# Kernel tuning notes

Measured on AMD Instinct MI355X. Metric: run time of the kernel, lower is better.

## Reference

```python
import jax, jax.numpy as jnp
import numpy as np

BN_EPS = 1e-5


def setup_inputs() -> dict:
    key = jax.random.key(0)
    ks = jax.random.split(key, 12)
    N, F, H, E, ED, G, EMB = 59392, 116, 256, 950272, 5, 8, 16
    return {
        "x": jax.random.normal(ks[0], (N, F), dtype=jnp.float32),
        "edge_index": jax.random.randint(ks[1], (2, E), 0, N, dtype=jnp.int64),
        "edge_attr": jax.random.normal(ks[2], (E, ED), dtype=jnp.float32),
        "group_ids": jax.random.randint(ks[3], (N,), 0, G, dtype=jnp.int64),
        "group_emb": jax.random.normal(ks[4], (G, EMB), dtype=jnp.float32),
        "W_in": jax.random.normal(ks[5], (F + EMB, H), dtype=jnp.float32) * 0.05,
        "b_in": jnp.zeros((H,), dtype=jnp.float32),
        "gamma": jnp.ones((H,), dtype=jnp.float32),
        "beta": jnp.zeros((H,), dtype=jnp.float32),
        "We": jax.random.normal(ks[6], (ED, H), dtype=jnp.float32) * 0.05,
        "be": jnp.zeros((H,), dtype=jnp.float32),
        "W1": jax.random.normal(ks[7], (H, H), dtype=jnp.float32) * 0.05,
        "b1": jnp.zeros((H,), dtype=jnp.float32),
        "W2": jax.random.normal(ks[8], (H, H), dtype=jnp.float32) * 0.05,
        "b2": jnp.zeros((H,), dtype=jnp.float32),
    }


def reference(x, edge_index, edge_attr, group_ids, group_emb, W_in, b_in,
              gamma, beta, We, be, W1, b1, W2, b2):
    N = x.shape[0]
    # group-embedding concat (dropout is identity in eval mode)
    h = jnp.concatenate([x, group_emb[group_ids]], axis=-1)      # [N, F+EMB]
    # dynamically-created Linear + ReLU
    h = jax.nn.relu(h @ W_in + b_in)                              # [N, H]
    # BatchNorm over nodes (training stats, biased var)
    mu = jnp.mean(h, axis=0)
    var = jnp.mean(jnp.square(h - mu), axis=0)
    h = (h - mu) * jax.lax.rsqrt(var + BN_EPS) * gamma + beta
    # GINEConv: msg = ReLU(x_j + lin(edge_attr)); sum-aggregate at target
    src, dst = edge_index[0], edge_index[1]
    msg = jax.nn.relu(h[src] + edge_attr @ We + be)               # [E, H]
    agg = jax.ops.segment_sum(msg, dst, num_segments=N)          # [N, H]
    z = h + agg                                                   # (1+eps)*h, eps=0
    out = jax.nn.relu(z @ W1 + b1) @ W2 + b2                      # 2-layer MLP
    out = jax.nn.relu(out)
    return (out, edge_attr)
```

## Files before the change

### kernel.cpp

```cpp
#include <hip/hip_runtime.h>
#include <hip/hip_bf16.h>
#include <cstdint>
#include <cstddef>

#define H 256
#define EMB 16
#define ED 5
#define BN_EPS 1e-5f

typedef __attribute__((ext_vector_type(8))) short short8;
typedef __attribute__((ext_vector_type(4))) float f32x4;
typedef _Float16 h2 __attribute__((ext_vector_type(2)));

__device__ __forceinline__ unsigned short f2bf(float f) {
  unsigned int u = __float_as_uint(f);
  unsigned int r = (u + 0x7fffu + ((u >> 16) & 1u)) >> 16;
  return (unsigned short)r;
}
__device__ __forceinline__ unsigned int pk2bf(float a, float b) {
  return (unsigned int)f2bf(a) | ((unsigned int)f2bf(b) << 16);
}
__device__ __forceinline__ float bfhi(unsigned int u) {
  return __uint_as_float(u & 0xffff0000u);
}
__device__ __forceinline__ float bflo(unsigned int u) {
  return __uint_as_float(u << 16);
}
__device__ __forceinline__ h2 u2h2(unsigned int u) {
  union { unsigned int u; h2 h; } c;
  c.u = u;
  return c.h;
}
__device__ __forceinline__ unsigned int h22u(h2 h) {
  union { h2 h; unsigned int u; } c;
  c.h = h;
  return c.u;
}
__device__ __forceinline__ h2 mkh2(float a, float b) {
  h2 r;
  r.x = (_Float16)a;
  r.y = (_Float16)b;
  return r;
}

__global__ __launch_bounds__(256) void prep_kernel(
    const float* __restrict__ Win, const float* __restrict__ W1,
    const float* __restrict__ W2, const float* __restrict__ gemb,
    const float* __restrict__ b_in, unsigned short* __restrict__ Wtx,
    unsigned short* __restrict__ Wt1, unsigned short* __restrict__ Wt2,
    float* __restrict__ T, float* __restrict__ stats, int* __restrict__ deg,
    int N, int F, int G) {
  int idx = blockIdx.x * 256 + threadIdx.x;
  if (idx < 1024) stats[idx] = 0.f;
  if (idx < N) deg[idx] = 0;
  if (idx < 256 * 128) {
    int n = idx >> 7, k = idx & 127;
    Wtx[idx] = f2bf((k < F) ? Win[(size_t)k * H + n] : 0.f);
  } else if (idx < 256 * 128 + 65536) {
    int i2 = idx - 256 * 128;
    int n = i2 >> 8, k = i2 & 255;
    Wt1[i2] = f2bf(W1[(size_t)k * H + n]);
  } else if (idx < 256 * 128 + 131072) {
    int i2 = idx - 256 * 128 - 65536;
    int n = i2 >> 8, k = i2 & 255;
    Wt2[i2] = f2bf(W2[(size_t)k * H + n]);
  } else if (idx < 256 * 128 + 131072 + G * 256) {
    int i2 = idx - 256 * 128 - 131072;
    int g = i2 >> 8, c = i2 & 255;
    float s = b_in[c];
    #pragma unroll
    for (int k = 0; k < EMB; ++k)
      s = fmaf(gemb[g * EMB + k], Win[(size_t)(F + k) * H + c], s);
    T[i2] = s;
  }
}

__global__ __launch_bounds__(256) void gemm_in_kernel(
    const float* __restrict__ x, const int* __restrict__ gid,
    const unsigned short* __restrict__ Wtx, const float* __restrict__ T,
    unsigned short* __restrict__ h0, float* __restrict__ stats, int F) {
  const int m0 = blockIdx.y * 128;
  const int n0 = blockIdx.x * 128;
  const int tid = threadIdx.x;
  const int lane = tid & 63;
  const int wave = tid >> 6;
  const int wm = (wave & 1) * 64;
  const int wn = (wave >> 1) * 64;
  const int l16 = lane & 15;
  const int quad = lane >> 4;
  __shared__ __align__(16) unsigned short As[128][40];
  __shared__ __align__(16) unsigned short Bs[128][40];
  __shared__ float cs[128], css[128];
  if (tid < 128) {
    cs[tid] = 0.f;
    css[tid] = 0.f;
  }
  f32x4 acc[4][4] = {};
  const int srow = tid >> 1;
  const int half = tid & 1;
  for (int k0 = 0; k0 < 128; k0 += 32) {
    __syncthreads();
    {
      const float* xp = x + (size_t)(m0 + srow) * F;
      float4 xv[4];
      #pragma unroll
      for (int f = 0; f < 4; ++f) {
        int c = k0 + half * 16 + f * 4;
        xv[f] = (c < F) ? *(const float4*)(xp + c)
                        : make_float4(0.f, 0.f, 0.f, 0.f);
      }
      uint4 p0, p1;
      p0.x = pk2bf(xv[0].x, xv[0].y); p0.y = pk2bf(xv[0].z, xv[0].w);
      p0.z = pk2bf(xv[1].x, xv[1].y); p0.w = pk2bf(xv[1].z, xv[1].w);
      p1.x = pk2bf(xv[2].x, xv[2].y); p1.y = pk2bf(xv[2].z, xv[2].w);
      p1.z = pk2bf(xv[3].x, xv[3].y); p1.w = pk2bf(xv[3].z, xv[3].w);
      *(uint4*)(&As[srow][half * 16]) = p0;
      *(uint4*)(&As[srow][half * 16 + 8]) = p1;
    }
    {
      const unsigned short* wp = Wtx + (size_t)(n0 + srow) * 128 + k0 + half * 16;
      *(uint4*)(&Bs[srow][half * 16]) = *(const uint4*)wp;
      *(uint4*)(&Bs[srow][half * 16 + 8]) = *(const uint4*)(wp + 8);
    }
    __syncthreads();
    short8 af[4], bf[4];
    #pragma unroll
    for (int i = 0; i < 4; ++i)
      af[i] = *(const short8*)(&As[wm + i * 16 + l16][quad * 8]);
    #pragma unroll
    for (int j = 0; j < 4; ++j)
      bf[j] = *(const short8*)(&Bs[wn + j * 16 + l16][quad * 8]);
    #pragma unroll
    for (int i = 0; i < 4; ++i)
      #pragma unroll
      for (int j = 0; j < 4; ++j)
        acc[i][j] = __builtin_amdgcn_mfma_f32_16x16x32_bf16(af[i], bf[j],
                                                            acc[i][j], 0, 0, 0);
  }
  int gi[4][4];
  #pragma unroll
  for (int i = 0; i < 4; ++i)
    #pragma unroll
    for (int r = 0; r < 4; ++r)
      gi[i][r] = gid[m0 + wm + i * 16 + quad * 4 + r];
  float ls[4] = {}, lss[4] = {};
  #pragma unroll
  for (int j = 0; j < 4; ++j) {
    const int col = n0 + wn + j * 16 + l16;
    #pragma unroll
    for (int i = 0; i < 4; ++i) {
      #pragma unroll
      for (int r = 0; r < 4; ++r) {
        const int row = m0 + wm + i * 16 + quad * 4 + r;
        float v = fmaxf(acc[i][j][r] + T[gi[i][r] * H + col], 0.f);
        h0[(size_t)row * H + col] = f2bf(v);
        ls[j] += v;
        lss[j] = fmaf(v, v, lss[j]);
      }
    }
  }
  #pragma unroll
  for (int j = 0; j < 4; ++j) {
    const int lc = wn + j * 16 + l16;
    atomicAdd(&cs[lc], ls[j]);
    atomicAdd(&css[lc], lss[j]);
  }
  __syncthreads();
  if (tid < 128) {
    atomicAdd(&stats[n0 + tid], cs[tid]);
    atomicAdd(&stats[H + n0 + tid], css[tid]);
  }
}

__global__ __launch_bounds__(256) void mlp_kernel(
    const unsigned short* __restrict__ z, const unsigned short* __restrict__ Wt1,
    const unsigned short* __restrict__ Wt2, const float* __restrict__ b1,
    const float* __restrict__ b2, float* __restrict__ out) {
  const int m0 = blockIdx.x * 64;
  const int tid = threadIdx.x;
  const int lane = tid & 63;
  const int wave = tid >> 6;
  const int wn = wave * 64;
  const int l16 = lane & 15;
  const int quad = lane >> 4;
  __shared__ __align__(16) unsigned short As[64][40];
  __shared__ __align__(16) unsigned short Bs[256][40];
  __shared__ __align__(16) unsigned short hidS[64][264];
  f32x4 acc[4][4] = {};
  const int ar = tid >> 2, ac = tid & 3;
  for (int k0 = 0; k0 < 256; k0 += 32) {
    __syncthreads();
    *(float4*)(&As[ar][ac * 8]) =
        *(const float4*)(z + (size_t)(m0 + ar) * H + k0 + ac * 8);
    #pragma unroll
    for (int t = 0; t < 4; ++t) {
      int r = ar + t * 64;
      *(float4*)(&Bs[r][ac * 8]) =
          *(const float4*)(Wt1 + (size_t)r * H + k0 + ac * 8);
    }
    __syncthreads();
    short8 af[4], bf[4];
    #pragma unroll
    for (int i = 0; i < 4; ++i)
      af[i] = *(const short8*)(&As[i * 16 + l16][quad * 8]);
    #pragma unroll
    for (int j = 0; j < 4; ++j)
      bf[j] = *(const short8*)(&Bs[wn + j * 16 + l16][quad * 8]);
    #pragma unroll
    for (int i = 0; i < 4; ++i)
      #pragma unroll
      for (int j = 0; j < 4; ++j)
        acc[i][j] = __builtin_amdgcn_mfma_f32_16x16x32_bf16(af[i], bf[j],
                                                            acc[i][j], 0, 0, 0);
  }
  #pragma unroll
  for (int j = 0; j < 4; ++j) {
    const int col = wn + j * 16 + l16;
    const float bj = b1[col];
    #pragma unroll
    for (int i = 0; i < 4; ++i)
      #pragma unroll
      for (int r = 0; r < 4; ++r) {
        const int row = i * 16 + quad * 4 + r;
        hidS[row][col] = f2bf(fmaxf(acc[i][j][r] + bj, 0.f));
      }
  }
  #pragma unroll
  for (int i = 0; i < 4; ++i)
    #pragma unroll
    for (int j = 0; j < 4; ++j)
      acc[i][j] = (f32x4){0.f, 0.f, 0.f, 0.f};
  for (int k0 = 0; k0 < 256; k0 += 32) {
    __syncthreads();
    #pragma unroll
    for (int t = 0; t < 4; ++t) {
      int r = ar + t * 64;
      *(float4*)(&Bs[r][ac * 8]) =
          *(const float4*)(Wt2 + (size_t)r * H + k0 + ac * 8);
    }
    __syncthreads();
    short8 af[4], bf[4];
    #pragma unroll
    for (int i = 0; i < 4; ++i)
      af[i] = *(const short8*)(&hidS[i * 16 + l16][k0 + quad * 8]);
    #pragma unroll
    for (int j = 0; j < 4; ++j)
      bf[j] = *(const short8*)(&Bs[wn + j * 16 + l16][quad * 8]);
    #pragma unroll
    for (int i = 0; i < 4; ++i)
      #pragma unroll
      for (int j = 0; j < 4; ++j)
        acc[i][j] = __builtin_amdgcn_mfma_f32_16x16x32_bf16(af[i], bf[j],
                                                            acc[i][j], 0, 0, 0);
  }
  #pragma unroll
  for (int j = 0; j < 4; ++j) {
    const int col = wn + j * 16 + l16;
    const float bj = b2[col];
    #pragma unroll
    for (int i = 0; i < 4; ++i)
      #pragma unroll
      for (int r = 0; r < 4; ++r) {
        const int row = m0 + i * 16 + quad * 4 + r;
        out[(size_t)row * H + col] = fmaxf(acc[i][j][r] + bj, 0.f);
      }
  }
}

__global__ __launch_bounds__(256) void hbn_kernel(
    const unsigned short* __restrict__ h0, const float* __restrict__ stats,
    const float* __restrict__ gamma, const float* __restrict__ beta,
    const float* __restrict__ be, unsigned short* __restrict__ hbn,
    float inv_n) {
  __shared__ float sa[H], sb[H];
  {
    const int j = threadIdx.x;
    const float mu = stats[j] * inv_n;
    const float var = stats[H + j] * inv_n - mu * mu;
    const float rs = 1.0f / sqrtf(var + BN_EPS);
    const float a = gamma[j] * rs;
    sa[j] = a;
    sb[j] = beta[j] - mu * a + be[j];
  }
  __syncthreads();
  const size_t i = (size_t)blockIdx.x * 256 + threadIdx.x;
  const int c = ((int)(i & 31)) * 8;
  const uint4 hv = ((const uint4*)h0)[i];
  float r[8] = {bflo(hv.x), bfhi(hv.x), bflo(hv.y), bfhi(hv.y),
                bflo(hv.z), bfhi(hv.z), bflo(hv.w), bfhi(hv.w)};
  float o[8];
  #pragma unroll
  for (int t = 0; t < 8; ++t)
    o[t] = fmaf(sa[c + t], r[t], sb[c + t]);
  uint4 ov;
  ov.x = h22u(mkh2(o[0], o[1]));
  ov.y = h22u(mkh2(o[2], o[3]));
  ov.z = h22u(mkh2(o[4], o[5]));
  ov.w = h22u(mkh2(o[6], o[7]));
  ((uint4*)hbn)[i] = ov;
}

__global__ __launch_bounds__(256) void csr_count_kernel(
    const int* __restrict__ ei, int* __restrict__ deg, int E) {
  int e = blockIdx.x * 256 + threadIdx.x;
  if (e < E) atomicAdd(&deg[ei[E + e]], 1);
}

__global__ __launch_bounds__(256) void scan_blocks_kernel(
    const int* __restrict__ deg, int* __restrict__ excl,
    int* __restrict__ bsums, int n) {
  const int tid = threadIdx.x;
  const int i = blockIdx.x * 256 + tid;
  const int lane = tid & 63, wid = tid >> 6;
  int v = (i < n) ? deg[i] : 0;
  int x = v;
  #pragma unroll
  for (int d = 1; d < 64; d <<= 1) {
    int y = __shfl_up(x, d, 64);
    if (lane >= d) x += y;
  }
  __shared__ int ws[4], wo[4];
  if (lane == 63) ws[wid] = x;
  __syncthreads();
  if (tid == 0) {
    int a = 0;
    #pragma unroll
    for (int w = 0; w < 4; ++w) { wo[w] = a; a += ws[w]; }
    bsums[blockIdx.x] = a;
  }
  __syncthreads();
  if (i < n) excl[i] = x - v + wo[wid];
}

__global__ __launch_bounds__(256) void scan_finish_kernel(
    int* __restrict__ row_start, int* __restrict__ cursor,
    const int* __restrict__ bsums, int n, int E, int NB) {
  const int tid = threadIdx.x;
  const int b = blockIdx.x;
  int v = (tid < b && tid < NB) ? bsums[tid] : 0;
  int s = v;
  #pragma unroll
  for (int d = 32; d > 0; d >>= 1) s += __shfl_down(s, d, 64);
  __shared__ int ws[4];
  if ((tid & 63) == 0) ws[tid >> 6] = s;
  __syncthreads();
  const int S = ws[0] + ws[1] + ws[2] + ws[3];
  const int i = b * 256 + tid;
  if (i < n) {
    int r = row_start[i] + S;
    row_start[i] = r;
    cursor[i] = r;
  }
  if (b == 0 && tid == 0) row_start[n] = E;
}

__global__ __launch_bounds__(256) void csr_scatter_kernel(
    const int* __restrict__ ei, const float* __restrict__ ea,
    int* __restrict__ cursor, uint4* __restrict__ rec,
    float* __restrict__ ea_out, int E) {
  int e = blockIdx.x * 256 + threadIdx.x;
  if (e >= E) return;
  int s = ei[e];
  int d = ei[E + e];
  int p = atomicAdd(&cursor[d], 1);
  const float* eap = ea + (size_t)e * ED;
  const float e0 = eap[0], e1 = eap[1], e2 = eap[2], e3 = eap[3], e4 = eap[4];
  uint4 r;
  r.x = (unsigned)s;
  r.y = h22u(mkh2(e0, e1));
  r.z = h22u(mkh2(e2, e3));
  r.w = h22u(mkh2(e4, 0.f));
  rec[p] = r;
  float* op = ea_out + (size_t)e * ED;
  op[0] = e0; op[1] = e1; op[2] = e2; op[3] = e3; op[4] = e4;
}

__device__ __forceinline__ void edge_accum(
    const uint4 rr, const uint2 hv, const h2 wA[5], const h2 wB[5],
    float& ax, float& ay, float& az, float& aw) {
  h2 m01 = u2h2(hv.x);
  h2 m23 = u2h2(hv.y);
  const h2 e01 = u2h2(rr.y), e23 = u2h2(rr.z), e44 = u2h2(rr.w);
  h2 t;
  t.x = e01.x; t.y = e01.x;  m01 += t * wA[0]; m23 += t * wB[0];
  t.x = e01.y; t.y = e01.y;  m01 += t * wA[1]; m23 += t * wB[1];
  t.x = e23.x; t.y = e23.x;  m01 += t * wA[2]; m23 += t * wB[2];
  t.x = e23.y; t.y = e23.y;  m01 += t * wA[3]; m23 += t * wB[3];
  t.x = e44.x; t.y = e44.x;  m01 += t * wA[4]; m23 += t * wB[4];
  const h2 z2 = {(_Float16)0.f, (_Float16)0.f};
  m01 = __builtin_elementwise_max(m01, z2);
  m23 = __builtin_elementwise_max(m23, z2);
  ax += (float)m01.x;
  ay += (float)m01.y;
  az += (float)m23.x;
  aw += (float)m23.y;
}

__global__ __launch_bounds__(256) void aggregate_kernel(
    const unsigned short* __restrict__ hbn, const uint4* __restrict__ rec,
    const float* __restrict__ We, const float* __restrict__ be,
    const int* __restrict__ row_start, unsigned short* __restrict__ z,
    int N) {
  const int lane = threadIdx.x & 63;
  int n = blockIdx.x * 4 + (threadIdx.x >> 6);
  if (n >= N) return;
  n = __builtin_amdgcn_readfirstlane(n);
  const int c = lane * 4;
  const float4 be4 = *(const float4*)(be + c);
  h2 wA[5], wB[5];
  #pragma unroll
  for (int k = 0; k < 5; ++k) {
    wA[k] = mkh2(We[k * H + c], We[k * H + c + 1]);
    wB[k] = mkh2(We[k * H + c + 2], We[k * H + c + 3]);
  }
  float ax = 0.f, ay = 0.f, az = 0.f, aw = 0.f;
  const int s0 = __builtin_amdgcn_readfirstlane(row_start[n]);
  const int s1 = __builtin_amdgcn_readfirstlane(row_start[n + 1]);
  const uint4* rp = rec + s0;
  const int cnt = s1 - s0;
  int i = 0;
  for (; i + 8 <= cnt; i += 8) {
    uint4 rr[8];
    uint2 hh[8];
    #pragma unroll
    for (int u = 0; u < 8; ++u) rr[u] = rp[i + u];
    #pragma unroll
    for (int u = 0; u < 8; ++u)
      hh[u] = *(const uint2*)(hbn + (size_t)(int)rr[u].x * H + c);
    #pragma unroll
    for (int u = 0; u < 8; ++u)
      edge_accum(rr[u], hh[u], wA, wB, ax, ay, az, aw);
  }
  for (; i + 4 <= cnt; i += 4) {
    uint4 rr[4];
    uint2 hh[4];
    #pragma unroll
    for (int u = 0; u < 4; ++u) rr[u] = rp[i + u];
    #pragma unroll
    for (int u = 0; u < 4; ++u)
      hh[u] = *(const uint2*)(hbn + (size_t)(int)rr[u].x * H + c);
    #pragma unroll
    for (int u = 0; u < 4; ++u)
      edge_accum(rr[u], hh[u], wA, wB, ax, ay, az, aw);
  }
  for (; i < cnt; ++i) {
    const uint4 r0 = rp[i];
    const uint2 h0v = *(const uint2*)(hbn + (size_t)(int)r0.x * H + c);
    edge_accum(r0, h0v, wA, wB, ax, ay, az, aw);
  }
  const uint2 hs = *(const uint2*)(hbn + (size_t)n * H + c);
  const h2 hsA = u2h2(hs.x), hsB = u2h2(hs.y);
  float zx = (float)hsA.x - be4.x + ax;
  float zy = (float)hsA.y - be4.y + ay;
  float zz = (float)hsB.x - be4.z + az;
  float zw = (float)hsB.y - be4.w + aw;
  uint2 o;
  o.x = pk2bf(zx, zy);
  o.y = pk2bf(zz, zw);
  *(uint2*)(z + (size_t)n * H + c) = o;
}

extern "C" void kernel_launch(void* const* d_in, const int* in_sizes, int n_in,
                              void* d_out, int out_size, void* d_ws, size_t ws_size,
                              hipStream_t stream) {
  const float* x     = (const float*)d_in[0];
  const int*   ei    = (const int*)d_in[1];
  const float* ea    = (const float*)d_in[2];
  const int*   gid   = (const int*)d_in[3];
  const float* gemb  = (const float*)d_in[4];
  const float* W_in  = (const float*)d_in[5];
  const float* b_in  = (const float*)d_in[6];
  const float* gamma = (const float*)d_in[7];
  const float* beta  = (const float*)d_in[8];
  const float* We    = (const float*)d_in[9];
  const float* be    = (const float*)d_in[10];
  const float* W1    = (const float*)d_in[11];
  const float* b1    = (const float*)d_in[12];
  const float* W2    = (const float*)d_in[13];
  const float* b2    = (const float*)d_in[14];
  float* out = (float*)d_out;

  const int N = in_sizes[3];
  const int E = in_sizes[1] / 2;
  const int F = in_sizes[0] / N;
  const int G = in_sizes[4] / EMB;
  const int NB = (N + 255) / 256;

  char* p = (char*)d_ws;
  auto take = [&](size_t bytes) {
    char* r = p;
    p += (bytes + 255) & ~(size_t)255;
    return r;
  };
  float* stats          = (float*)take(1024 * sizeof(float));
  int* deg              = (int*)take((size_t)N * 4);
  int* row_start        = (int*)take((size_t)(N + 1) * 4);
  int* cursor           = (int*)take((size_t)N * 4);
  int* bsums            = (int*)take((size_t)NB * 4);
  uint4* rec            = (uint4*)take((size_t)E * 16);
  unsigned short* Wtx   = (unsigned short*)take((size_t)256 * 128 * 2);
  unsigned short* Wt1   = (unsigned short*)take((size_t)H * H * 2);
  unsigned short* Wt2   = (unsigned short*)take((size_t)H * H * 2);
  float* T              = (float*)take((size_t)G * H * 4);
  unsigned short* h0    = (unsigned short*)take((size_t)N * H * 2);
  unsigned short* hbn   = (unsigned short*)take((size_t)N * H * 2);
  unsigned short* z     = (unsigned short*)take((size_t)N * H * 2);

  {
    int total = 256 * 128 + 131072 + G * 256;
    int nb = (total + 255) / 256;
    if (nb < (N + 255) / 256) nb = (N + 255) / 256;
    prep_kernel<<<nb, 256, 0, stream>>>(W_in, W1, W2, gemb, b_in, Wtx, Wt1,
                                        Wt2, T, stats, deg, N, F, G);
  }

  csr_count_kernel<<<(E + 255) / 256, 256, 0, stream>>>(ei, deg, E);
  scan_blocks_kernel<<<NB, 256, 0, stream>>>(deg, row_start, bsums, N);
  scan_finish_kernel<<<NB, 256, 0, stream>>>(row_start, cursor, bsums, N, E, NB);
  csr_scatter_kernel<<<(E + 255) / 256, 256, 0, stream>>>(
      ei, ea, cursor, rec, out + (size_t)N * H, E);

  dim3 ggrid(H / 128, N / 128);
  gemm_in_kernel<<<ggrid, 256, 0, stream>>>(x, gid, Wtx, T, h0, stats, F);

  hbn_kernel<<<((size_t)N * H / 8) / 256, 256, 0, stream>>>(
      h0, stats, gamma, beta, be, hbn, 1.0f / (float)N);

  aggregate_kernel<<<(N + 3) / 4, 256, 0, stream>>>(hbn, rec, We, be,
                                                    row_start, z, N);

  mlp_kernel<<<N / 64, 256, 0, stream>>>(z, Wt1, Wt2, b1, b2, out);
}
```

Measured before the change: 391.6 us.

## Split each node's edge list across two waves and pre-shift source offsets

The aggregate kernel now gives each destination node two wavefronts, each handling half of its incoming edges, and sums the partials through shared memory before writing z. The CSR record stores the source index pre-multiplied by the row byte stride, which removes the 64-bit multiply in the gather address. The tail loops are replaced by one clamped, predicated 8-wide loop. This aims to raise memory-level parallelism and shorten the serial per-node chain, at the cost of a block barrier, shared-memory traffic, wasted clamped loads and twice as many waves.

```diff
diff --git a/kernel.cpp b/kernel.cpp
--- a/kernel.cpp
+++ b/kernel.cpp
@@ -366,7 +366,7 @@
   const float* eap = ea + (size_t)e * ED;
   const float e0 = eap[0], e1 = eap[1], e2 = eap[2], e3 = eap[3], e4 = eap[4];
   uint4 r;
-  r.x = (unsigned)s;
+  r.x = ((unsigned)s) << 9;
   r.y = h22u(mkh2(e0, e1));
   r.z = h22u(mkh2(e2, e3));
   r.w = h22u(mkh2(e4, 0.f));
@@ -401,12 +401,16 @@
     const float* __restrict__ We, const float* __restrict__ be,
     const int* __restrict__ row_start, unsigned short* __restrict__ z,
     int N) {
-  const int lane = threadIdx.x & 63;
-  int n = blockIdx.x * 4 + (threadIdx.x >> 6);
-  if (n >= N) return;
-  n = __builtin_amdgcn_readfirstlane(n);
+  __shared__ float sAgg[2][256];
+  const int tid = threadIdx.x;
+  const int lane = tid & 63;
+  const int wave = tid >> 6;
+  const int nl = wave >> 1;
+  const int half = wave & 1;
+  const int n0 = blockIdx.x * 2 + nl;
+  const int n = __builtin_amdgcn_readfirstlane((n0 < N) ? n0 : (N - 1));
   const int c = lane * 4;
-  const float4 be4 = *(const float4*)(be + c);
+  const int c2 = c << 1;
   h2 wA[5], wB[5];
   #pragma unroll
   for (int k = 0; k < 5; ++k) {
@@ -416,48 +420,48 @@
   float ax = 0.f, ay = 0.f, az = 0.f, aw = 0.f;
   const int s0 = __builtin_amdgcn_readfirstlane(row_start[n]);
   const int s1 = __builtin_amdgcn_readfirstlane(row_start[n + 1]);
+  const int cnt = s1 - s0;
+  const int mid = cnt >> 1;
+  int i = half ? mid : 0;
+  const int e = half ? cnt : mid;
   const uint4* rp = rec + s0;
-  const int cnt = s1 - s0;
-  int i = 0;
-  for (; i + 8 <= cnt; i += 8) {
+  const char* hb = (const char*)hbn;
+  for (; i < e; i += 8) {
     uint4 rr[8];
     uint2 hh[8];
     #pragma unroll
-    for (int u = 0; u < 8; ++u) rr[u] = rp[i + u];
+    for (int u = 0; u < 8; ++u) {
+      int idx = i + u;
+      idx = (idx < e) ? idx : (e - 1);
+      rr[u] = rp[idx];
+    }
     #pragma unroll
     for (int u = 0; u < 8; ++u)
-      hh[u] = *(const uint2*)(hbn + (size_t)(int)rr[u].x * H + c);
+      hh[u] = *(const uint2*)(hb + rr[u].x + c2);
+    asm volatile("" ::: "memory");
     #pragma unroll
     for (int u = 0; u < 8; ++u)
-      edge_accum(rr[u], hh[u], wA, wB, ax, ay, az, aw);
-  }
-  for (; i + 4 <= cnt; i += 4) {
-    uint4 rr[4];
-    uint2 hh[4];
-    #pragma unroll
-    for (int u = 0; u < 4; ++u) rr[u] = rp[i + u];
-    #pragma unroll
-    for (int u = 0; u < 4; ++u)
-      hh[u] = *(const uint2*)(hbn + (size_t)(int)rr[u].x * H + c);
-    #pragma unroll
-    for (int u = 0; u < 4; ++u)
-      edge_accum(rr[u], hh[u], wA, wB, ax, ay, az, aw);
-  }
-  for (; i < cnt; ++i) {
-    const uint4 r0 = rp[i];
-    const uint2 h0v = *(const uint2*)(hbn + (size_t)(int)r0.x * H + c);
-    edge_accum(r0, h0v, wA, wB, ax, ay, az, aw);
-  }
-  const uint2 hs = *(const uint2*)(hbn + (size_t)n * H + c);
-  const h2 hsA = u2h2(hs.x), hsB = u2h2(hs.y);
-  float zx = (float)hsA.x - be4.x + ax;
-  float zy = (float)hsA.y - be4.y + ay;
-  float zz = (float)hsB.x - be4.z + az;
-  float zw = (float)hsB.y - be4.w + aw;
-  uint2 o;
-  o.x = pk2bf(zx, zy);
-  o.y = pk2bf(zz, zw);
-  *(uint2*)(z + (size_t)n * H + c) = o;
+      if (i + u < e)
+        edge_accum(rr[u], hh[u], wA, wB, ax, ay, az, aw);
+  }
+  if (half) {
+    *(float4*)(&sAgg[nl][c]) = make_float4(ax, ay, az, aw);
+  }
+  __syncthreads();
+  if (!half && n0 < N) {
+    const float4 p = *(const float4*)(&sAgg[nl][c]);
+    const float4 be4 = *(const float4*)(be + c);
+    const uint2 hs = *(const uint2*)(hbn + (size_t)n * H + c);
+    const h2 hsA = u2h2(hs.x), hsB = u2h2(hs.y);
+    const float zx = (float)hsA.x - be4.x + ax + p.x;
+    const float zy = (float)hsA.y - be4.y + ay + p.y;
+    const float zz = (float)hsB.x - be4.z + az + p.z;
+    const float zw = (float)hsB.y - be4.w + aw + p.w;
+    uint2 o;
+    o.x = pk2bf(zx, zy);
+    o.y = pk2bf(zz, zw);
+    *(uint2*)(z + (size_t)n * H + c) = o;
+  }
 }
 
 extern "C" void kernel_launch(void* const* d_in, const int* in_sizes, int n_in,
@@ -526,7 +530,7 @@
   hbn_kernel<<<((size_t)N * H / 8) / 256, 256, 0, stream>>>(
       h0, stats, gamma, beta, be, hbn, 1.0f / (float)N);
 
-  aggregate_kernel<<<(N + 3) / 4, 256, 0, stream>>>(hbn, rec, We, be,
+  aggregate_kernel<<<(N + 1) / 2, 256, 0, stream>>>(hbn, rec, We, be,
                                                     row_start, z, N);
 
   mlp_kernel<<<N / 64, 256, 0, stream>>>(z, Wt1, Wt2, b1, b2, out);
```

Measured after the change: 435.6 us. +11.2%, slower.

## Software-pipeline edge gathers and precompute byte offsets in aggregate kernel

Applied to the files above, without the earlier changes.

The CSR scatter now stores each source index as a byte offset (index shifted by 9, i.e. times 512 bytes per row), so gather addresses in the aggregate kernel need no multiply or 64-bit conversion. The aggregate loop is double-buffered: the next batch of 8 records and feature gathers is issued before computing the current batch, with scheduling barriers to keep loads ahead of the math. A vector-zero trick forces vector loads for row_start and the records. This is meant to hide gather latency at the cost of more registers; the shifted offsets fit in 32 bits only because N*512 is below 2^32.

```diff
diff --git a/kernel.cpp b/kernel.cpp
--- a/kernel.cpp
+++ b/kernel.cpp
@@ -366,7 +366,7 @@
   const float* eap = ea + (size_t)e * ED;
   const float e0 = eap[0], e1 = eap[1], e2 = eap[2], e3 = eap[3], e4 = eap[4];
   uint4 r;
-  r.x = (unsigned)s;
+  r.x = ((unsigned)s) << 9;
   r.y = h22u(mkh2(e0, e1));
   r.z = h22u(mkh2(e2, e3));
   r.w = h22u(mkh2(e4, 0.f));
@@ -396,6 +396,19 @@
   aw += (float)m23.y;
 }
 
+#define LOADB8(rr, hh, base)                                      \
+  {                                                               \
+    _Pragma("unroll") for (int u = 0; u < 8; ++u)                 \
+        rr[u] = rp[(base) + u];                                   \
+    _Pragma("unroll") for (int u = 0; u < 8; ++u)                 \
+        hh[u] = *(const uint2*)(hb + rr[u].x + c2);               \
+  }
+#define COMP8(rr, hh)                                             \
+  {                                                               \
+    _Pragma("unroll") for (int u = 0; u < 8; ++u)                 \
+        edge_accum(rr[u], hh[u], wA, wB, ax, ay, az, aw);         \
+  }
+
 __global__ __launch_bounds__(256) void aggregate_kernel(
     const unsigned short* __restrict__ hbn, const uint4* __restrict__ rec,
     const float* __restrict__ We, const float* __restrict__ be,
@@ -406,6 +419,9 @@
   if (n >= N) return;
   n = __builtin_amdgcn_readfirstlane(n);
   const int c = lane * 4;
+  const int c2 = c << 1;
+  int vzero;
+  asm("v_mov_b32 %0, 0" : "=v"(vzero));
   const float4 be4 = *(const float4*)(be + c);
   h2 wA[5], wB[5];
   #pragma unroll
@@ -414,22 +430,32 @@
     wB[k] = mkh2(We[k * H + c + 2], We[k * H + c + 3]);
   }
   float ax = 0.f, ay = 0.f, az = 0.f, aw = 0.f;
-  const int s0 = __builtin_amdgcn_readfirstlane(row_start[n]);
-  const int s1 = __builtin_amdgcn_readfirstlane(row_start[n + 1]);
-  const uint4* rp = rec + s0;
+  const int2 rs2 = *(const int2*)(row_start + n + vzero);
+  const int s0 = __builtin_amdgcn_readfirstlane(rs2.x);
+  const int s1 = __builtin_amdgcn_readfirstlane(rs2.y);
   const int cnt = s1 - s0;
-  int i = 0;
-  for (; i + 8 <= cnt; i += 8) {
-    uint4 rr[8];
-    uint2 hh[8];
-    #pragma unroll
-    for (int u = 0; u < 8; ++u) rr[u] = rp[i + u];
-    #pragma unroll
-    for (int u = 0; u < 8; ++u)
-      hh[u] = *(const uint2*)(hbn + (size_t)(int)rr[u].x * H + c);
-    #pragma unroll
-    for (int u = 0; u < 8; ++u)
-      edge_accum(rr[u], hh[u], wA, wB, ax, ay, az, aw);
+  const uint4* rp = rec + s0 + vzero;
+  const char* hb = (const char*)hbn;
+  const int nb = cnt >> 3;
+  int i = nb << 3;
+  if (nb > 0) {
+    uint4 rrA[8], rrB[8];
+    uint2 hhA[8], hhB[8];
+    LOADB8(rrA, hhA, 0);
+    for (int b = 1; b < nb; ++b) {
+      if (b & 1) {
+        LOADB8(rrB, hhB, b << 3);
+        __builtin_amdgcn_sched_barrier(0);
+        COMP8(rrA, hhA);
+      } else {
+        LOADB8(rrA, hhA, b << 3);
+        __builtin_amdgcn_sched_barrier(0);
+        COMP8(rrB, hhB);
+      }
+    }
+    __builtin_amdgcn_sched_barrier(0);
+    if (nb & 1) { COMP8(rrA, hhA); }
+    else        { COMP8(rrB, hhB); }
   }
   for (; i + 4 <= cnt; i += 4) {
     uint4 rr[4];
@@ -438,14 +464,14 @@
     for (int u = 0; u < 4; ++u) rr[u] = rp[i + u];
     #pragma unroll
     for (int u = 0; u < 4; ++u)
-      hh[u] = *(const uint2*)(hbn + (size_t)(int)rr[u].x * H + c);
+      hh[u] = *(const uint2*)(hb + rr[u].x + c2);
     #pragma unroll
     for (int u = 0; u < 4; ++u)
       edge_accum(rr[u], hh[u], wA, wB, ax, ay, az, aw);
   }
   for (; i < cnt; ++i) {
     const uint4 r0 = rp[i];
-    const uint2 h0v = *(const uint2*)(hbn + (size_t)(int)r0.x * H + c);
+    const uint2 h0v = *(const uint2*)(hb + r0.x + c2);
     edge_accum(r0, h0v, wA, wB, ax, ay, az, aw);
   }
   const uint2 hs = *(const uint2*)(hbn + (size_t)n * H + c);
```

After: 462.9 us. 18.2% more time.

## Fuse BatchNorm apply into edge aggregation and drop the hbn pass

Applied to the files above, without the earlier changes.

Removes the separate hbn kernel. gemm_in now stores h0 in fp16, and aggregate_kernel recomputes the per-column BN scale and shift from stats and applies them to each gathered neighbour row on the fly. That saves a full N×H read and write plus one launch, at the cost of a few extra fp16 FMAs per edge. The edge record now holds a pre-shifted byte offset to drop address arithmetic, and the edge_attr output copy moves out of the scatter kernel into a separate vectorised copy kernel. Applying the affine in fp16 on fp16-stored h0 may change numerics slightly.

```diff
diff --git a/kernel.cpp b/kernel.cpp
--- a/kernel.cpp
+++ b/kernel.cpp
@@ -20,11 +20,10 @@
 __device__ __forceinline__ unsigned int pk2bf(float a, float b) {
   return (unsigned int)f2bf(a) | ((unsigned int)f2bf(b) << 16);
 }
-__device__ __forceinline__ float bfhi(unsigned int u) {
-  return __uint_as_float(u & 0xffff0000u);
-}
-__device__ __forceinline__ float bflo(unsigned int u) {
-  return __uint_as_float(u << 16);
+__device__ __forceinline__ unsigned short f2h(float f) {
+  union { _Float16 h; unsigned short u; } c;
+  c.h = (_Float16)f;
+  return c.u;
 }
 __device__ __forceinline__ h2 u2h2(unsigned int u) {
   union { unsigned int u; h2 h; } c;
@@ -153,7 +152,7 @@
       for (int r = 0; r < 4; ++r) {
         const int row = m0 + wm + i * 16 + quad * 4 + r;
         float v = fmaxf(acc[i][j][r] + T[gi[i][r] * H + col], 0.f);
-        h0[(size_t)row * H + col] = f2bf(v);
+        h0[(size_t)row * H + col] = f2h(v);
         ls[j] += v;
         lss[j] = fmaf(v, v, lss[j]);
       }
@@ -267,39 +266,6 @@
   }
 }
 
-__global__ __launch_bounds__(256) void hbn_kernel(
-    const unsigned short* __restrict__ h0, const float* __restrict__ stats,
-    const float* __restrict__ gamma, const float* __restrict__ beta,
-    const float* __restrict__ be, unsigned short* __restrict__ hbn,
-    float inv_n) {
-  __shared__ float sa[H], sb[H];
-  {
-    const int j = threadIdx.x;
-    const float mu = stats[j] * inv_n;
-    const float var = stats[H + j] * inv_n - mu * mu;
-    const float rs = 1.0f / sqrtf(var + BN_EPS);
-    const float a = gamma[j] * rs;
-    sa[j] = a;
-    sb[j] = beta[j] - mu * a + be[j];
-  }
-  __syncthreads();
-  const size_t i = (size_t)blockIdx.x * 256 + threadIdx.x;
-  const int c = ((int)(i & 31)) * 8;
-  const uint4 hv = ((const uint4*)h0)[i];
-  float r[8] = {bflo(hv.x), bfhi(hv.x), bflo(hv.y), bfhi(hv.y),
-                bflo(hv.z), bfhi(hv.z), bflo(hv.w), bfhi(hv.w)};
-  float o[8];
-  #pragma unroll
-  for (int t = 0; t < 8; ++t)
-    o[t] = fmaf(sa[c + t], r[t], sb[c + t]);
-  uint4 ov;
-  ov.x = h22u(mkh2(o[0], o[1]));
-  ov.y = h22u(mkh2(o[2], o[3]));
-  ov.z = h22u(mkh2(o[4], o[5]));
-  ov.w = h22u(mkh2(o[6], o[7]));
-  ((uint4*)hbn)[i] = ov;
-}
-
 __global__ __launch_bounds__(256) void csr_count_kernel(
     const int* __restrict__ ei, int* __restrict__ deg, int E) {
   int e = blockIdx.x * 256 + threadIdx.x;
@@ -356,8 +322,7 @@
 
 __global__ __launch_bounds__(256) void csr_scatter_kernel(
     const int* __restrict__ ei, const float* __restrict__ ea,
-    int* __restrict__ cursor, uint4* __restrict__ rec,
-    float* __restrict__ ea_out, int E) {
+    int* __restrict__ cursor, uint4* __restrict__ rec, int E) {
   int e = blockIdx.x * 256 + threadIdx.x;
   if (e >= E) return;
   int s = ei[e];
@@ -366,20 +331,30 @@
   const float* eap = ea + (size_t)e * ED;
   const float e0 = eap[0], e1 = eap[1], e2 = eap[2], e3 = eap[3], e4 = eap[4];
   uint4 r;
-  r.x = (unsigned)s;
+  r.x = ((unsigned)s) << 9;
   r.y = h22u(mkh2(e0, e1));
   r.z = h22u(mkh2(e2, e3));
   r.w = h22u(mkh2(e4, 0.f));
   rec[p] = r;
-  float* op = ea_out + (size_t)e * ED;
-  op[0] = e0; op[1] = e1; op[2] = e2; op[3] = e3; op[4] = e4;
+}
+
+__global__ __launch_bounds__(256) void ea_copy_kernel(
+    const float* __restrict__ in, float* __restrict__ out, int W) {
+  int i = blockIdx.x * 256 + threadIdx.x;
+  int i4 = i * 4;
+  if (i4 + 3 < W) {
+    *(float4*)(out + i4) = *(const float4*)(in + i4);
+  } else if (i4 < W) {
+    for (int k = 0; k < 4 && i4 + k < W; ++k) out[i4 + k] = in[i4 + k];
+  }
 }
 
 __device__ __forceinline__ void edge_accum(
-    const uint4 rr, const uint2 hv, const h2 wA[5], const h2 wB[5],
+    const uint4 rr, const uint2 hv, const h2 aA, const h2 aB,
+    const h2 bA, const h2 bB, const h2 wA[5], const h2 wB[5],
     float& ax, float& ay, float& az, float& aw) {
-  h2 m01 = u2h2(hv.x);
-  h2 m23 = u2h2(hv.y);
+  h2 m01 = aA * u2h2(hv.x) + bA;
+  h2 m23 = aB * u2h2(hv.y) + bB;
   const h2 e01 = u2h2(rr.y), e23 = u2h2(rr.z), e44 = u2h2(rr.w);
   h2 t;
   t.x = e01.x; t.y = e01.x;  m01 += t * wA[0]; m23 += t * wB[0];
@@ -397,16 +372,38 @@
 }
 
 __global__ __launch_bounds__(256) void aggregate_kernel(
-    const unsigned short* __restrict__ hbn, const uint4* __restrict__ rec,
+    const unsigned short* __restrict__ h0, const uint4* __restrict__ rec,
     const float* __restrict__ We, const float* __restrict__ be,
-    const int* __restrict__ row_start, unsigned short* __restrict__ z,
-    int N) {
+    const float* __restrict__ gamma, const float* __restrict__ beta,
+    const float* __restrict__ stats, const int* __restrict__ row_start,
+    unsigned short* __restrict__ z, int N, float inv_n) {
   const int lane = threadIdx.x & 63;
   int n = blockIdx.x * 4 + (threadIdx.x >> 6);
   if (n >= N) return;
   n = __builtin_amdgcn_readfirstlane(n);
   const int c = lane * 4;
+  const int c2 = c << 1;
   const float4 be4 = *(const float4*)(be + c);
+  h2 aA, aB, bA, bB;
+  {
+    const float4 s1v = *(const float4*)(stats + c);
+    const float4 s2v = *(const float4*)(stats + H + c);
+    const float4 g4 = *(const float4*)(gamma + c);
+    const float4 bt4 = *(const float4*)(beta + c);
+    float a[4], b[4];
+    float m0 = s1v.x * inv_n, m1 = s1v.y * inv_n,
+          m2 = s1v.z * inv_n, m3 = s1v.w * inv_n;
+    a[0] = g4.x / sqrtf(s2v.x * inv_n - m0 * m0 + BN_EPS);
+    a[1] = g4.y / sqrtf(s2v.y * inv_n - m1 * m1 + BN_EPS);
+    a[2] = g4.z / sqrtf(s2v.z * inv_n - m2 * m2 + BN_EPS);
+    a[3] = g4.w / sqrtf(s2v.w * inv_n - m3 * m3 + BN_EPS);
+    b[0] = bt4.x - m0 * a[0] + be4.x;
+    b[1] = bt4.y - m1 * a[1] + be4.y;
+    b[2] = bt4.z - m2 * a[2] + be4.z;
+    b[3] = bt4.w - m3 * a[3] + be4.w;
+    aA = mkh2(a[0], a[1]); aB = mkh2(a[2], a[3]);
+    bA = mkh2(b[0], b[1]); bB = mkh2(b[2], b[3]);
+  }
   h2 wA[5], wB[5];
   #pragma unroll
   for (int k = 0; k < 5; ++k) {
@@ -418,6 +415,7 @@
   const int s1 = __builtin_amdgcn_readfirstlane(row_start[n + 1]);
   const uint4* rp = rec + s0;
   const int cnt = s1 - s0;
+  const char* hb = (const char*)h0;
   int i = 0;
   for (; i + 8 <= cnt; i += 8) {
     uint4 rr[8];
@@ -426,10 +424,10 @@
     for (int u = 0; u < 8; ++u) rr[u] = rp[i + u];
     #pragma unroll
     for (int u = 0; u < 8; ++u)
-      hh[u] = *(const uint2*)(hbn + (size_t)(int)rr[u].x * H + c);
+      hh[u] = *(const uint2*)(hb + rr[u].x + c2);
     #pragma unroll
     for (int u = 0; u < 8; ++u)
-      edge_accum(rr[u], hh[u], wA, wB, ax, ay, az, aw);
+      edge_accum(rr[u], hh[u], aA, aB, bA, bB, wA, wB, ax, ay, az, aw);
   }
   for (; i + 4 <= cnt; i += 4) {
     uint4 rr[4];
@@ -438,22 +436,23 @@
     for (int u = 0; u < 4; ++u) rr[u] = rp[i + u];
     #pragma unroll
     for (int u = 0; u < 4; ++u)
-      hh[u] = *(const uint2*)(hbn + (size_t)(int)rr[u].x * H + c);
+      hh[u] = *(const uint2*)(hb + rr[u].x + c2);
     #pragma unroll
     for (int u = 0; u < 4; ++u)
-      edge_accum(rr[u], hh[u], wA, wB, ax, ay, az, aw);
+      edge_accum(rr[u], hh[u], aA, aB, bA, bB, wA, wB, ax, ay, az, aw);
   }
   for (; i < cnt; ++i) {
     const uint4 r0 = rp[i];
-    const uint2 h0v = *(const uint2*)(hbn + (size_t)(int)r0.x * H + c);
-    edge_accum(r0, h0v, wA, wB, ax, ay, az, aw);
-  }
-  const uint2 hs = *(const uint2*)(hbn + (size_t)n * H + c);
-  const h2 hsA = u2h2(hs.x), hsB = u2h2(hs.y);
-  float zx = (float)hsA.x - be4.x + ax;
-  float zy = (float)hsA.y - be4.y + ay;
-  float zz = (float)hsB.x - be4.z + az;
-  float zw = (float)hsB.y - be4.w + aw;
+    const uint2 h0v = *(const uint2*)(hb + r0.x + c2);
+    edge_accum(r0, h0v, aA, aB, bA, bB, wA, wB, ax, ay, az, aw);
+  }
+  const uint2 hs = *(const uint2*)(h0 + (size_t)n * H + c);
+  const h2 s01 = aA * u2h2(hs.x) + bA;
+  const h2 s23 = aB * u2h2(hs.y) + bB;
+  float zx = (float)s01.x - be4.x + ax;
+  float zy = (float)s01.y - be4.y + ay;
+  float zz = (float)s23.x - be4.z + az;
+  float zw = (float)s23.y - be4.w + aw;
   uint2 o;
   o.x = pk2bf(zx, zy);
   o.y = pk2bf(zz, zw);
@@ -497,13 +496,12 @@
   int* row_start        = (int*)take((size_t)(N + 1) * 4);
   int* cursor           = (int*)take((size_t)N * 4);
   int* bsums            = (int*)take((size_t)NB * 4);
-  uint4* rec            = (uint4*)take((size_t)E * 16);
+  uint4* rec            = (uint4*)take((size_t)(E + 1) * 16);
   unsigned short* Wtx   = (unsigned short*)take((size_t)256 * 128 * 2);
   unsigned short* Wt1   = (unsigned short*)take((size_t)H * H * 2);
   unsigned short* Wt2   = (unsigned short*)take((size_t)H * H * 2);
   float* T              = (float*)take((size_t)G * H * 4);
   unsigned short* h0    = (unsigned short*)take((size_t)N * H * 2);
-  unsigned short* hbn   = (unsigned short*)take((size_t)N * H * 2);
   unsigned short* z     = (unsigned short*)take((size_t)N * H * 2);
 
   {
@@ -517,17 +515,18 @@
   csr_count_kernel<<<(E + 255) / 256, 256, 0, stream>>>(ei, deg, E);
   scan_blocks_kernel<<<NB, 256, 0, stream>>>(deg, row_start, bsums, N);
   scan_finish_kernel<<<NB, 256, 0, stream>>>(row_start, cursor, bsums, N, E, NB);
-  csr_scatter_kernel<<<(E + 255) / 256, 256, 0, stream>>>(
-      ei, ea, cursor, rec, out + (size_t)N * H, E);
+  csr_scatter_kernel<<<(E + 255) / 256, 256, 0, stream>>>(ei, ea, cursor, rec, E);
+  {
+    int W = E * ED;
+    int nb = (W / 4 + 255) / 256 + 1;
+    ea_copy_kernel<<<nb, 256, 0, stream>>>(ea, out + (size_t)N * H, W);
+  }
 
   dim3 ggrid(H / 128, N / 128);
   gemm_in_kernel<<<ggrid, 256, 0, stream>>>(x, gid, Wtx, T, h0, stats, F);
 
-  hbn_kernel<<<((size_t)N * H / 8) / 256, 256, 0, stream>>>(
-      h0, stats, gamma, beta, be, hbn, 1.0f / (float)N);
-
-  aggregate_kernel<<<(N + 3) / 4, 256, 0, stream>>>(hbn, rec, We, be,
-                                                    row_start, z, N);
+  aggregate_kernel<<<(N + 3) / 4, 256, 0, stream>>>(
+      h0, rec, We, be, gamma, beta, stats, row_start, z, N, 1.0f / (float)N);
 
   mlp_kernel<<<N / 64, 256, 0, stream>>>(z, Wt1, Wt2, b1, b2, out);
 }
```

After: 387.1 us. No clear change (-1.1%).
